# Kernel optimization log

Hardware: AMD Instinct MI355X
Metric: run time of the kernel (lower is better)

Reference implementation:

```python
import jax, jax.numpy as jnp
import numpy as np

N = 4096      # mesh nodes (seq len)
D = 512       # input_dim_nodes / hidden_size
F = 512       # ffn_hidden_size (hidden_dim)
NH = 4        # num_attention_heads
HD = D // NH  # head dim = 128
L = 2         # processor_layers
EPS = 1e-5
SCALE = 1.0 / float(np.sqrt(HD))
NEG = -1e9


def setup_inputs() -> dict:
    key = jax.random.key(0)
    ks = jax.random.split(key, 16)
    nfeat = jax.random.normal(ks[0], (N, D), jnp.float32)
    # sparse graph adjacency mask: True = masked out (TE 'arbitrary' convention)
    mask = jax.random.uniform(ks[1], (N, N)) < 0.99
    idx = jnp.arange(N)
    mask = mask.at[idx, idx].set(False)  # keep self-edges unmasked
    s = 0.02
    p = lambda k, shape: jax.random.normal(k, shape, jnp.float32) * s
    return dict(
        nfeat=nfeat, mask=mask,
        ln1_g=jnp.ones((L, D), jnp.float32), ln1_b=jnp.zeros((L, D), jnp.float32),
        wq=p(ks[2], (L, D, D)), bq=p(ks[3], (L, D)),
        wk=p(ks[4], (L, D, D)), bk=p(ks[5], (L, D)),
        wv=p(ks[6], (L, D, D)), bv=p(ks[7], (L, D)),
        wo=p(ks[8], (L, D, D)), bo=p(ks[9], (L, D)),
        ln2_g=jnp.ones((L, D), jnp.float32), ln2_b=jnp.zeros((L, D), jnp.float32),
        fc1_w=p(ks[10], (L, F, D)), fc1_b=p(ks[11], (L, F)),
        fc2_w=p(ks[12], (L, D, F)), fc2_b=p(ks[13], (L, D)),
    )


def _ln(x, g, b):
    mu = x.mean(-1, keepdims=True)
    var = ((x - mu) ** 2).mean(-1, keepdims=True)
    return (x - mu) * jax.lax.rsqrt(var + EPS) * g + b


def reference(nfeat, mask, ln1_g, ln1_b, wq, bq, wk, bk, wv, bv, wo, bo,
              ln2_g, ln2_b, fc1_w, fc1_b, fc2_w, fc2_b):
    def layer(x, p):
        g1, b1, Wq, Bq, Wk, Bk, Wv, Bv, Wo, Bo, g2, b2, W1, B1, W2, B2 = p
        # --- pre-LN self-attention with arbitrary mask ---
        h = _ln(x, g1, b1)                                  # [N, D]
        q = (h @ Wq.T + Bq).reshape(N, NH, HD)
        k = (h @ Wk.T + Bk).reshape(N, NH, HD)
        v = (h @ Wv.T + Bv).reshape(N, NH, HD)
        scores = jnp.einsum('qhd,khd->hqk', q, k) * SCALE   # [NH, N, N]
        scores = jnp.where(mask[None], NEG, scores)
        attn = jax.nn.softmax(scores, axis=-1)
        o = jnp.einsum('hqk,khd->qhd', attn, v).reshape(N, D)
        x = x + o @ Wo.T + Bo
        # --- pre-LN MLP ---
        h2 = _ln(x, g2, b2)
        m = jax.nn.gelu(h2 @ W1.T + B1, approximate=False) @ W2.T + B2
        return x + m, None

    xs = (ln1_g, ln1_b, wq, bq, wk, bk, wv, bv, wo, bo,
          ln2_g, ln2_b, fc1_w, fc1_b, fc2_w, fc2_b)
    out, _ = jax.lax.scan(layer, nfeat, xs)
    return out
```

## Files before the change

kernel.cpp:

```cpp
#include <hip/hip_runtime.h>
#include <math.h>

#define NN 4096
#define DD 512
#define FF 512
#define NHEAD 4
#define HDIM 128
#define CAP 256
#define SCALE 0.08838834764831845f

typedef __attribute__((ext_vector_type(8))) short short8;
typedef __attribute__((ext_vector_type(8))) unsigned short ushort8;
typedef __attribute__((ext_vector_type(4))) unsigned short ushort4v;
typedef __attribute__((ext_vector_type(4))) float floatx4;

__device__ __forceinline__ float bf2f(unsigned short u) {
    union { unsigned int i; float f; } x; x.i = ((unsigned int)u) << 16; return x.f;
}
__device__ __forceinline__ unsigned short f2bf(float f) {
    union { float f; unsigned int i; } x; x.f = f;
    unsigned int r = (x.i + 0x7FFFu + ((x.i >> 16) & 1u)) >> 16;
    return (unsigned short)r;
}
__device__ __forceinline__ void gld_lds16(const void* g, void* l) {
    __builtin_amdgcn_global_load_lds((const __attribute__((address_space(1))) void*)g,
                                     (__attribute__((address_space(3))) void*)l, 16, 0, 0);
}

__global__ void build_idx_kernel(const int* __restrict__ mask,
                                 int* __restrict__ idx, int* __restrict__ cnt) {
    int row = blockIdx.x;
    __shared__ int c;
    if (threadIdx.x == 0) c = 0;
    __syncthreads();
    const int4* mrow = (const int4*)(mask + (size_t)row * NN);
    for (int j4 = threadIdx.x; j4 < NN / 4; j4 += blockDim.x) {
        int4 m4 = mrow[j4];
        int base = j4 * 4;
        if (m4.x == 0) idx[row * CAP + atomicAdd(&c, 1)] = base;
        if (m4.y == 0) idx[row * CAP + atomicAdd(&c, 1)] = base + 1;
        if (m4.z == 0) idx[row * CAP + atomicAdd(&c, 1)] = base + 2;
        if (m4.w == 0) idx[row * CAP + atomicAdd(&c, 1)] = base + 3;
    }
    __syncthreads();
    if (threadIdx.x == 0) cnt[row] = (c < CAP) ? c : CAP;
}

struct W6 { const float* w[6]; };
__global__ void cast_weights(W6 wp, unsigned short* __restrict__ dst) {
    int region = blockIdx.x >> 4;
    int layer = region / 6, mat = region - layer * 6;
    const float* src = wp.w[mat] + (size_t)layer * (DD * DD);
    unsigned short* d = dst + (size_t)region * (DD * DD);
    int off = (blockIdx.x & 15) * 16384 + threadIdx.x * 4;
#pragma unroll
    for (int i = 0; i < 16; i++) {
        int e = off + i * 1024;
        float4 f = *(const float4*)&src[e];
        ushort4v u;
        u.x = f2bf(f.x); u.y = f2bf(f.y); u.z = f2bf(f.z); u.w = f2bf(f.w);
        *(ushort4v*)&d[e] = u;
    }
}

__global__ void concat_bias(const float* __restrict__ bq, const float* __restrict__ bk,
                            const float* __restrict__ bv, float* __restrict__ bcat) {
    int l = blockIdx.x, t = threadIdx.x;
    bcat[l * 1536 + t]        = bq[l * 512 + t];
    bcat[l * 1536 + 512 + t]  = bk[l * 512 + t];
    bcat[l * 1536 + 1024 + t] = bv[l * 512 + t];
}

__global__ void ln_kernel(const float* __restrict__ x, const float* __restrict__ g,
                          const float* __restrict__ b, unsigned short* __restrict__ out) {
    int wave = threadIdx.x >> 6, lane = threadIdx.x & 63;
    int row = blockIdx.x * 4 + wave;
    const float* xr = x + (size_t)row * DD;
    float v[8];
    float4 p0 = *(const float4*)&xr[lane * 8];
    float4 p1 = *(const float4*)&xr[lane * 8 + 4];
    v[0] = p0.x; v[1] = p0.y; v[2] = p0.z; v[3] = p0.w;
    v[4] = p1.x; v[5] = p1.y; v[6] = p1.z; v[7] = p1.w;
    float s = 0.f;
#pragma unroll
    for (int i = 0; i < 8; i++) s += v[i];
#pragma unroll
    for (int off = 32; off; off >>= 1) s += __shfl_xor(s, off);
    float mu = s * (1.0f / DD);
    float vs = 0.f;
#pragma unroll
    for (int i = 0; i < 8; i++) { float d = v[i] - mu; vs += d * d; }
#pragma unroll
    for (int off = 32; off; off >>= 1) vs += __shfl_xor(vs, off);
    float r = rsqrtf(vs * (1.0f / DD) + 1e-5f);
    float4 g0 = *(const float4*)&g[lane * 8];
    float4 g1 = *(const float4*)&g[lane * 8 + 4];
    float4 b0 = *(const float4*)&b[lane * 8];
    float4 b1 = *(const float4*)&b[lane * 8 + 4];
    float ge[8] = {g0.x, g0.y, g0.z, g0.w, g1.x, g1.y, g1.z, g1.w};
    float be[8] = {b0.x, b0.y, b0.z, b0.w, b1.x, b1.y, b1.z, b1.w};
    ushort8 ov;
#pragma unroll
    for (int i = 0; i < 8; i++) ov[i] = f2bf((v[i] - mu) * r * ge[i] + be[i]);
    *(ushort8*)&out[(size_t)row * DD + lane * 8] = ov;
}

template <int MODE>
__launch_bounds__(256)
__global__ void gemm_bf16(const unsigned short* __restrict__ A, const unsigned short* __restrict__ B,
                          const float* __restrict__ bias, const float* __restrict__ resIn,
                          float* __restrict__ resOut, unsigned short* __restrict__ outB,
                          int M, int Nout, int K) {
    __shared__ unsigned short As[64 * 32];
    __shared__ unsigned short Bs[64 * 32];
    const int m0 = blockIdx.y * 64, n0 = blockIdx.x * 64;
    const int t = threadIdx.x;
    const int wave = t >> 6, lane = t & 63;
    const int wm = (wave & 1) * 32, wn = (wave >> 1) * 32;
    const int srow = t >> 2, scol = (t & 3) * 8;
    const int fr = lane & 15, fq = (lane >> 4) * 8;

    floatx4 acc[2][2] = {};

    const unsigned short* ag = A + (size_t)(m0 + srow) * K + scol;
    const unsigned short* bg = B + (size_t)(n0 + srow) * K + scol;
    unsigned short* as = As + t * 8;
    unsigned short* bs = Bs + t * 8;

    for (int k0 = 0; k0 < K; k0 += 32) {
        __syncthreads();
        gld_lds16(ag + k0, as);
        gld_lds16(bg + k0, bs);
        __syncthreads();
        short8 af[2], bf[2];
#pragma unroll
        for (int i = 0; i < 2; i++)
            af[i] = *(const short8*)&As[(wm + 16 * i + fr) * 32 + fq];
#pragma unroll
        for (int j = 0; j < 2; j++)
            bf[j] = *(const short8*)&Bs[(wn + 16 * j + fr) * 32 + fq];
#pragma unroll
        for (int i = 0; i < 2; i++)
#pragma unroll
            for (int j = 0; j < 2; j++)
                acc[i][j] = __builtin_amdgcn_mfma_f32_16x16x32_bf16(af[i], bf[j], acc[i][j], 0, 0, 0);
    }

    const int er = (lane >> 4) * 4, ec = lane & 15;
#pragma unroll
    for (int i = 0; i < 2; i++) {
#pragma unroll
        for (int j = 0; j < 2; j++) {
            int col = n0 + wn + 16 * j + ec;
            float bsv = bias[col];
#pragma unroll
            for (int r = 0; r < 4; r++) {
                int row = m0 + wm + 16 * i + er + r;
                float val = acc[i][j][r] + bsv;
                if (MODE == 1) val = 0.5f * val * (1.0f + erff(val * 0.70710678118654752f));
                if (MODE == 2) {
                    resOut[(size_t)row * Nout + col] = resIn[(size_t)row * Nout + col] + val;
                } else {
                    outB[(size_t)row * Nout + col] = f2bf(val);
                }
            }
        }
    }
}

__global__ void sparse_attn(const unsigned short* __restrict__ qkv, const int* __restrict__ idx,
                            const int* __restrict__ cnt, unsigned short* __restrict__ o) {
    int wave = threadIdx.x >> 6, lane = threadIdx.x & 63;
    int qslot = wave >> 1, half = wave & 1;
    int qi = blockIdx.x * 4 + qslot;
    __shared__ float obuf[4][64][8];
    __shared__ float sbuf[4][64];

    ushort8 qv = *(const ushort8*)(qkv + (size_t)qi * 1536 + lane * 8);
    float qf[8];
#pragma unroll
    for (int e = 0; e < 8; e++) qf[e] = bf2f(qv[e]);

    int c = cnt[qi];
    const int* ir = idx + qi * CAP;
    float sum = 0.f, oa[8] = {};

    for (int j = half; j < c; j += 2) {
        int kj = ir[j];
        const unsigned short* kv_base = qkv + (size_t)kj * 1536;
        ushort8 kv = *(const ushort8*)(kv_base + 512 + lane * 8);
        ushort8 vv = *(const ushort8*)(kv_base + 1024 + lane * 8);
        float d = 0.f;
#pragma unroll
        for (int e = 0; e < 8; e++) d += qf[e] * bf2f(kv[e]);
        d += __shfl_xor(d, 1);
        d += __shfl_xor(d, 2);
        d += __shfl_xor(d, 4);
        d += __shfl_xor(d, 8);
        float p = __expf(d * SCALE);
        sum += p;
#pragma unroll
        for (int e = 0; e < 8; e++) oa[e] += p * bf2f(vv[e]);
    }

    if (half == 1) {
#pragma unroll
        for (int e = 0; e < 8; e++) obuf[qslot][lane][e] = oa[e];
        sbuf[qslot][lane] = sum;
    }
    __syncthreads();
    if (half == 0) {
        sum += sbuf[qslot][lane];
        float inv = 1.0f / sum;
        ushort8 ov;
#pragma unroll
        for (int e = 0; e < 8; e++) ov[e] = f2bf((oa[e] + obuf[qslot][lane][e]) * inv);
        *(ushort8*)(o + (size_t)qi * 512 + lane * 8) = ov;
    }
}

extern "C" void kernel_launch(void* const* d_in, const int* in_sizes, int n_in,
                              void* d_out, int out_size, void* d_ws, size_t ws_size,
                              hipStream_t stream) {
    const float* nfeat = (const float*)d_in[0];
    const int*   mask  = (const int*)d_in[1];
    const float* ln1_g = (const float*)d_in[2];
    const float* ln1_b = (const float*)d_in[3];
    const float* wq    = (const float*)d_in[4];
    const float* bq    = (const float*)d_in[5];
    const float* wk    = (const float*)d_in[6];
    const float* bk    = (const float*)d_in[7];
    const float* wv    = (const float*)d_in[8];
    const float* bv    = (const float*)d_in[9];
    const float* wo    = (const float*)d_in[10];
    const float* bo    = (const float*)d_in[11];
    const float* ln2_g = (const float*)d_in[12];
    const float* ln2_b = (const float*)d_in[13];
    const float* fc1_w = (const float*)d_in[14];
    const float* fc1_b = (const float*)d_in[15];
    const float* fc2_w = (const float*)d_in[16];
    const float* fc2_b = (const float*)d_in[17];

    const size_t ND = (size_t)NN * DD;
    float* x            = (float*)d_ws;
    unsigned short* h   = (unsigned short*)(x + ND);
    unsigned short* qkv = h + ND;
    unsigned short* o   = qkv + (size_t)NN * 1536;
    unsigned short* m1  = o + ND;
    unsigned short* wc  = m1 + ND;
    float* bcat         = (float*)(wc + (size_t)12 * DD * DD);
    int*   idx          = (int*)(bcat + 2 * 1536);
    int*   cnt          = idx + (size_t)NN * CAP;

    W6 w6;
    w6.w[0] = wq; w6.w[1] = wk; w6.w[2] = wv; w6.w[3] = wo; w6.w[4] = fc1_w; w6.w[5] = fc2_w;
    cast_weights<<<192, 256, 0, stream>>>(w6, wc);
    concat_bias<<<2, 512, 0, stream>>>(bq, bk, bv, bcat);
    build_idx_kernel<<<NN, 256, 0, stream>>>(mask, idx, cnt);

    for (int l = 0; l < 2; l++) {
        size_t bOff = (size_t)l * DD;
        unsigned short* wl = wc + (size_t)l * 6 * DD * DD;
        const float* xin = (l == 0) ? nfeat : x;
        float* fc2_dst = (l == 1) ? (float*)d_out : x;

        ln_kernel<<<NN / 4, 256, 0, stream>>>(xin, ln1_g + bOff, ln1_b + bOff, h);
        gemm_bf16<0><<<dim3(24, 64), 256, 0, stream>>>(h, wl, bcat + l * 1536, nullptr, nullptr, qkv, NN, 1536, DD);
        sparse_attn<<<NN / 4, 512, 0, stream>>>(qkv, idx, cnt, o);
        gemm_bf16<2><<<dim3(8, 64), 256, 0, stream>>>(o, wl + (size_t)3 * DD * DD, bo + bOff, xin, x, nullptr, NN, DD, DD);
        ln_kernel<<<NN / 4, 256, 0, stream>>>(x, ln2_g + bOff, ln2_b + bOff, h);
        gemm_bf16<1><<<dim3(8, 64), 256, 0, stream>>>(h, wl + (size_t)4 * DD * DD, fc1_b + bOff, nullptr, nullptr, m1, NN, FF, DD);
        gemm_bf16<2><<<dim3(8, 64), 256, 0, stream>>>(m1, wl + (size_t)5 * DD * DD, fc2_b + bOff, x, fc2_dst, nullptr, NN, DD, FF);
    }
}
```

Baseline: 309.4 us.

## Fold LayerNorm into GEMM weights and compute row stats in residual epilogues

Folds the LayerNorm gamma/beta into the bf16 QKV and FC1 weights, adding per-column constants c0/c1, so the standalone LN kernels disappear. Row sum and sum-of-squares come from an init kernel for the input and from atomics in the residual-GEMM epilogues, which also write a bf16 copy of x. The following GEMM then applies mean/rstd in its epilogue. This removes four LN launches and their extra passes over x, in exchange for atomics, a one-pass variance formula with possible cancellation error, and bf16 rounding of the unnormalized x.

```diff
diff --git a/kernel.cpp b/kernel.cpp
--- a/kernel.cpp
+++ b/kernel.cpp
@@ -4,14 +4,11 @@
 #define NN 4096
 #define DD 512
 #define FF 512
-#define NHEAD 4
-#define HDIM 128
 #define CAP 256
 #define SCALE 0.08838834764831845f
 
 typedef __attribute__((ext_vector_type(8))) short short8;
 typedef __attribute__((ext_vector_type(8))) unsigned short ushort8;
-typedef __attribute__((ext_vector_type(4))) unsigned short ushort4v;
 typedef __attribute__((ext_vector_type(4))) float floatx4;
 
 __device__ __forceinline__ float bf2f(unsigned short u) {
@@ -46,71 +43,91 @@
     if (threadIdx.x == 0) cnt[row] = (c < CAP) ? c : CAP;
 }
 
-struct W6 { const float* w[6]; };
-__global__ void cast_weights(W6 wp, unsigned short* __restrict__ dst) {
-    int region = blockIdx.x >> 4;
-    int layer = region / 6, mat = region - layer * 6;
-    const float* src = wp.w[mat] + (size_t)layer * (DD * DD);
-    unsigned short* d = dst + (size_t)region * (DD * DD);
-    int off = (blockIdx.x & 15) * 16384 + threadIdx.x * 4;
-#pragma unroll
-    for (int i = 0; i < 16; i++) {
-        int e = off + i * 1024;
-        float4 f = *(const float4*)&src[e];
-        ushort4v u;
-        u.x = f2bf(f.x); u.y = f2bf(f.y); u.z = f2bf(f.z); u.w = f2bf(f.w);
-        *(ushort4v*)&d[e] = u;
-    }
-}
-
-__global__ void concat_bias(const float* __restrict__ bq, const float* __restrict__ bk,
-                            const float* __restrict__ bv, float* __restrict__ bcat) {
-    int l = blockIdx.x, t = threadIdx.x;
-    bcat[l * 1536 + t]        = bq[l * 512 + t];
-    bcat[l * 1536 + 512 + t]  = bk[l * 512 + t];
-    bcat[l * 1536 + 1024 + t] = bv[l * 512 + t];
-}
-
-__global__ void ln_kernel(const float* __restrict__ x, const float* __restrict__ g,
-                          const float* __restrict__ b, unsigned short* __restrict__ out) {
+struct FoldArgs {
+    const float* w[6];
+    const float* bias[6];
+    const float* ln1_g; const float* ln1_b;
+    const float* ln2_g; const float* ln2_b;
+};
+__global__ void fold_weights(FoldArgs fa, unsigned short* __restrict__ wc,
+                             float* __restrict__ c0, float* __restrict__ c1) {
+    int r = blockIdx.y;
+    int l = r / 6, m = r - l * 6;
+    int wave = threadIdx.x >> 6, lane = threadIdx.x & 63;
+    int n = blockIdx.x * 4 + wave;
+
+    const float* wrow = fa.w[m] + (size_t)l * DD * DD + (size_t)n * DD;
+    float4 w0 = *(const float4*)&wrow[lane * 8];
+    float4 w1 = *(const float4*)&wrow[lane * 8 + 4];
+    float we[8] = {w0.x, w0.y, w0.z, w0.w, w1.x, w1.y, w1.z, w1.w};
+
+    bool folded = (m < 3) || (m == 4);
+    float s1 = 0.f, sb = 0.f;
+    float wg[8];
+    if (folded) {
+        const float* gp = (m < 3) ? fa.ln1_g + l * DD : fa.ln2_g + l * DD;
+        const float* bp = (m < 3) ? fa.ln1_b + l * DD : fa.ln2_b + l * DD;
+        float4 g0 = *(const float4*)&gp[lane * 8];
+        float4 g1 = *(const float4*)&gp[lane * 8 + 4];
+        float4 b0 = *(const float4*)&bp[lane * 8];
+        float4 b1 = *(const float4*)&bp[lane * 8 + 4];
+        float ge[8] = {g0.x, g0.y, g0.z, g0.w, g1.x, g1.y, g1.z, g1.w};
+        float be[8] = {b0.x, b0.y, b0.z, b0.w, b1.x, b1.y, b1.z, b1.w};
+#pragma unroll
+        for (int e = 0; e < 8; e++) {
+            wg[e] = we[e] * ge[e];
+            s1 += wg[e];
+            sb += we[e] * be[e];
+        }
+    } else {
+#pragma unroll
+        for (int e = 0; e < 8; e++) wg[e] = we[e];
+    }
+    ushort8 ov;
+#pragma unroll
+    for (int e = 0; e < 8; e++) ov[e] = f2bf(wg[e]);
+    *(ushort8*)&wc[(size_t)r * DD * DD + (size_t)n * DD + lane * 8] = ov;
+
+    if (folded) {
+#pragma unroll
+        for (int off = 32; off; off >>= 1) { s1 += __shfl_xor(s1, off); sb += __shfl_xor(sb, off); }
+    }
+    if (lane == 0) {
+        c1[r * DD + n] = folded ? s1 : 0.f;
+        c0[r * DD + n] = (folded ? sb : 0.f) + fa.bias[m][l * DD + n];
+    }
+}
+
+__global__ void init_stats(const float* __restrict__ x, unsigned short* __restrict__ xb,
+                           float* __restrict__ S) {
     int wave = threadIdx.x >> 6, lane = threadIdx.x & 63;
     int row = blockIdx.x * 4 + wave;
     const float* xr = x + (size_t)row * DD;
-    float v[8];
     float4 p0 = *(const float4*)&xr[lane * 8];
     float4 p1 = *(const float4*)&xr[lane * 8 + 4];
-    v[0] = p0.x; v[1] = p0.y; v[2] = p0.z; v[3] = p0.w;
-    v[4] = p1.x; v[5] = p1.y; v[6] = p1.z; v[7] = p1.w;
-    float s = 0.f;
-#pragma unroll
-    for (int i = 0; i < 8; i++) s += v[i];
-#pragma unroll
-    for (int off = 32; off; off >>= 1) s += __shfl_xor(s, off);
-    float mu = s * (1.0f / DD);
-    float vs = 0.f;
-#pragma unroll
-    for (int i = 0; i < 8; i++) { float d = v[i] - mu; vs += d * d; }
-#pragma unroll
-    for (int off = 32; off; off >>= 1) vs += __shfl_xor(vs, off);
-    float r = rsqrtf(vs * (1.0f / DD) + 1e-5f);
-    float4 g0 = *(const float4*)&g[lane * 8];
-    float4 g1 = *(const float4*)&g[lane * 8 + 4];
-    float4 b0 = *(const float4*)&b[lane * 8];
-    float4 b1 = *(const float4*)&b[lane * 8 + 4];
-    float ge[8] = {g0.x, g0.y, g0.z, g0.w, g1.x, g1.y, g1.z, g1.w};
-    float be[8] = {b0.x, b0.y, b0.z, b0.w, b1.x, b1.y, b1.z, b1.w};
+    float v[8] = {p0.x, p0.y, p0.z, p0.w, p1.x, p1.y, p1.z, p1.w};
+    float s = 0.f, q = 0.f;
     ushort8 ov;
 #pragma unroll
-    for (int i = 0; i < 8; i++) ov[i] = f2bf((v[i] - mu) * r * ge[i] + be[i]);
-    *(ushort8*)&out[(size_t)row * DD + lane * 8] = ov;
+    for (int e = 0; e < 8; e++) { s += v[e]; q += v[e] * v[e]; ov[e] = f2bf(v[e]); }
+#pragma unroll
+    for (int off = 32; off; off >>= 1) { s += __shfl_xor(s, off); q += __shfl_xor(q, off); }
+    *(ushort8*)&xb[(size_t)row * DD + lane * 8] = ov;
+    if (lane == 0) { S[2 * row] = s; S[2 * row + 1] = q; }
+}
+
+__global__ void zero_kernel(float* __restrict__ p, int n) {
+    int i = blockIdx.x * blockDim.x + threadIdx.x;
+    if (i < n) p[i] = 0.f;
 }
 
 template <int MODE>
 __launch_bounds__(256)
 __global__ void gemm_bf16(const unsigned short* __restrict__ A, const unsigned short* __restrict__ B,
-                          const float* __restrict__ bias, const float* __restrict__ resIn,
+                          const float* __restrict__ c0, const float* __restrict__ c1,
+                          const float* __restrict__ statsIn, const float* __restrict__ resIn,
                           float* __restrict__ resOut, unsigned short* __restrict__ outB,
-                          int M, int Nout, int K) {
+                          float* __restrict__ statsOut, int M, int Nout, int K) {
     __shared__ unsigned short As[64 * 32];
     __shared__ unsigned short Bs[64 * 32];
     const int m0 = blockIdx.y * 64, n0 = blockIdx.x * 64;
@@ -147,21 +164,51 @@
     }
 
     const int er = (lane >> 4) * 4, ec = lane & 15;
+    int colj[2]; float c0v[2], c1v[2];
+#pragma unroll
+    for (int j = 0; j < 2; j++) {
+        colj[j] = n0 + wn + 16 * j + ec;
+        c0v[j] = c0[colj[j]];
+        if (MODE < 2) c1v[j] = c1[colj[j]];
+    }
+
 #pragma unroll
     for (int i = 0; i < 2; i++) {
 #pragma unroll
-        for (int j = 0; j < 2; j++) {
-            int col = n0 + wn + 16 * j + ec;
-            float bsv = bias[col];
-#pragma unroll
-            for (int r = 0; r < 4; r++) {
-                int row = m0 + wm + 16 * i + er + r;
-                float val = acc[i][j][r] + bsv;
-                if (MODE == 1) val = 0.5f * val * (1.0f + erff(val * 0.70710678118654752f));
+        for (int r = 0; r < 4; r++) {
+            int row = m0 + wm + 16 * i + er + r;
+            if (MODE < 2) {
+                float s = statsIn[2 * row], q = statsIn[2 * row + 1];
+                float mu = s * (1.0f / DD);
+                float var = q * (1.0f / DD) - mu * mu;
+                float rm = rsqrtf(var + 1e-5f);
+                float rmu = rm * mu;
+#pragma unroll
+                for (int j = 0; j < 2; j++) {
+                    float val = rm * acc[i][j][r] - rmu * c1v[j] + c0v[j];
+                    if (MODE == 1) val = 0.5f * val * (1.0f + erff(val * 0.70710678118654752f));
+                    outB[(size_t)row * Nout + colj[j]] = f2bf(val);
+                }
+            } else {
+                float xn[2];
+#pragma unroll
+                for (int j = 0; j < 2; j++) {
+                    xn[j] = resIn[(size_t)row * Nout + colj[j]] + acc[i][j][r] + c0v[j];
+                    resOut[(size_t)row * Nout + colj[j]] = xn[j];
+                    if (MODE == 2) outB[(size_t)row * Nout + colj[j]] = f2bf(xn[j]);
+                }
                 if (MODE == 2) {
-                    resOut[(size_t)row * Nout + col] = resIn[(size_t)row * Nout + col] + val;
-                } else {
-                    outB[(size_t)row * Nout + col] = f2bf(val);
+                    float s = xn[0] + xn[1];
+                    float q = xn[0] * xn[0] + xn[1] * xn[1];
+#pragma unroll
+                    for (int off = 1; off < 16; off <<= 1) {
+                        s += __shfl_xor(s, off);
+                        q += __shfl_xor(q, off);
+                    }
+                    if ((lane & 15) == 0) {
+                        atomicAdd(&statsOut[2 * row], s);
+                        atomicAdd(&statsOut[2 * row + 1], q);
+                    }
                 }
             }
         }
@@ -243,33 +290,48 @@
 
     const size_t ND = (size_t)NN * DD;
     float* x            = (float*)d_ws;
-    unsigned short* h   = (unsigned short*)(x + ND);
-    unsigned short* qkv = h + ND;
+    unsigned short* xb  = (unsigned short*)(x + ND);
+    unsigned short* qkv = xb + ND;
     unsigned short* o   = qkv + (size_t)NN * 1536;
     unsigned short* m1  = o + ND;
     unsigned short* wc  = m1 + ND;
-    float* bcat         = (float*)(wc + (size_t)12 * DD * DD);
-    int*   idx          = (int*)(bcat + 2 * 1536);
+    float* c0           = (float*)(wc + (size_t)12 * DD * DD);
+    float* c1           = c0 + 12 * DD;
+    float* S            = c1 + 12 * DD;
+    int*   idx          = (int*)(S + 4 * NN * 2);
     int*   cnt          = idx + (size_t)NN * CAP;
 
-    W6 w6;
-    w6.w[0] = wq; w6.w[1] = wk; w6.w[2] = wv; w6.w[3] = wo; w6.w[4] = fc1_w; w6.w[5] = fc2_w;
-    cast_weights<<<192, 256, 0, stream>>>(w6, wc);
-    concat_bias<<<2, 512, 0, stream>>>(bq, bk, bv, bcat);
+    FoldArgs fa;
+    fa.w[0] = wq; fa.w[1] = wk; fa.w[2] = wv; fa.w[3] = wo; fa.w[4] = fc1_w; fa.w[5] = fc2_w;
+    fa.bias[0] = bq; fa.bias[1] = bk; fa.bias[2] = bv; fa.bias[3] = bo; fa.bias[4] = fc1_b; fa.bias[5] = fc2_b;
+    fa.ln1_g = ln1_g; fa.ln1_b = ln1_b; fa.ln2_g = ln2_g; fa.ln2_b = ln2_b;
+
+    fold_weights<<<dim3(128, 12), 256, 0, stream>>>(fa, wc, c0, c1);
     build_idx_kernel<<<NN, 256, 0, stream>>>(mask, idx, cnt);
+    init_stats<<<NN / 4, 256, 0, stream>>>(nfeat, xb, S);
+    zero_kernel<<<24, 1024, 0, stream>>>(S + NN * 2, 3 * NN * 2);
 
     for (int l = 0; l < 2; l++) {
-        size_t bOff = (size_t)l * DD;
         unsigned short* wl = wc + (size_t)l * 6 * DD * DD;
-        const float* xin = (l == 0) ? nfeat : x;
-        float* fc2_dst = (l == 1) ? (float*)d_out : x;
-
-        ln_kernel<<<NN / 4, 256, 0, stream>>>(xin, ln1_g + bOff, ln1_b + bOff, h);
-        gemm_bf16<0><<<dim3(24, 64), 256, 0, stream>>>(h, wl, bcat + l * 1536, nullptr, nullptr, qkv, NN, 1536, DD);
+        float* cl0 = c0 + l * 6 * DD;
+        float* cl1 = c1 + l * 6 * DD;
+        float* Sa = S + (size_t)(2 * l) * NN * 2;
+        float* Sb = S + (size_t)(2 * l + 1) * NN * 2;
+        const float* resIn0 = (l == 0) ? nfeat : x;
+
+        gemm_bf16<0><<<dim3(24, 64), 256, 0, stream>>>(xb, wl, cl0, cl1, Sa,
+                                                       nullptr, nullptr, qkv, nullptr, NN, 1536, DD);
         sparse_attn<<<NN / 4, 512, 0, stream>>>(qkv, idx, cnt, o);
-        gemm_bf16<2><<<dim3(8, 64), 256, 0, stream>>>(o, wl + (size_t)3 * DD * DD, bo + bOff, xin, x, nullptr, NN, DD, DD);
-        ln_kernel<<<NN / 4, 256, 0, stream>>>(x, ln2_g + bOff, ln2_b + bOff, h);
-        gemm_bf16<1><<<dim3(8, 64), 256, 0, stream>>>(h, wl + (size_t)4 * DD * DD, fc1_b + bOff, nullptr, nullptr, m1, NN, FF, DD);
-        gemm_bf16<2><<<dim3(8, 64), 256, 0, stream>>>(m1, wl + (size_t)5 * DD * DD, fc2_b + bOff, x, fc2_dst, nullptr, NN, DD, FF);
-    }
-}
+        gemm_bf16<2><<<dim3(8, 64), 256, 0, stream>>>(o, wl + (size_t)3 * DD * DD, cl0 + 3 * DD, nullptr,
+                                                      nullptr, resIn0, x, xb, Sb, NN, DD, DD);
+        gemm_bf16<1><<<dim3(8, 64), 256, 0, stream>>>(xb, wl + (size_t)4 * DD * DD, cl0 + 4 * DD, cl1 + 4 * DD, Sb,
+                                                      nullptr, nullptr, m1, nullptr, NN, FF, DD);
+        if (l == 0) {
+            gemm_bf16<2><<<dim3(8, 64), 256, 0, stream>>>(m1, wl + (size_t)5 * DD * DD, cl0 + 5 * DD, nullptr,
+                                                          nullptr, x, x, xb, S + (size_t)2 * NN * 2, NN, DD, FF);
+        } else {
+            gemm_bf16<3><<<dim3(8, 64), 256, 0, stream>>>(m1, wl + (size_t)5 * DD * DD, cl0 + 5 * DD, nullptr,
+                                                          nullptr, x, (float*)d_out, nullptr, nullptr, NN, DD, FF);
+        }
+    }
+}
```

Result: slower. 321.8 us (+4.0%).

## Enlarge GEMM tiles and merge setup kernels into one launch

Applied to the files above, without the earlier changes.

The GEMM kernel now uses 128-row tiles with either 128 or 64 columns (templated NJ), so each wave computes a 64xN block with more MFMAs per LDS load and fewer blocks are launched. The weight cast, bias concat and mask-to-index build are folded into a single setup kernel that handles 8 mask rows per block, which cuts launch count and the per-row block overhead. The index build also gains a bounds check on CAP. The larger tiles raise register and LDS use per block and halve the grid size, which may reduce occupancy and load balance.

```diff
diff --git a/kernel.cpp b/kernel.cpp
--- a/kernel.cpp
+++ b/kernel.cpp
@@ -4,83 +4,91 @@
 #define NN 4096
 #define DD 512
 #define FF 512
-#define NHEAD 4
-#define HDIM 128
 #define CAP 256
 #define SCALE 0.08838834764831845f
 
+typedef unsigned short u16;
 typedef __attribute__((ext_vector_type(8))) short short8;
 typedef __attribute__((ext_vector_type(8))) unsigned short ushort8;
 typedef __attribute__((ext_vector_type(4))) unsigned short ushort4v;
 typedef __attribute__((ext_vector_type(4))) float floatx4;
 
-__device__ __forceinline__ float bf2f(unsigned short u) {
+__device__ __forceinline__ float bf2f(u16 u) {
     union { unsigned int i; float f; } x; x.i = ((unsigned int)u) << 16; return x.f;
 }
-__device__ __forceinline__ unsigned short f2bf(float f) {
+__device__ __forceinline__ u16 f2bf(float f) {
     union { float f; unsigned int i; } x; x.f = f;
     unsigned int r = (x.i + 0x7FFFu + ((x.i >> 16) & 1u)) >> 16;
-    return (unsigned short)r;
+    return (u16)r;
 }
 __device__ __forceinline__ void gld_lds16(const void* g, void* l) {
     __builtin_amdgcn_global_load_lds((const __attribute__((address_space(1))) void*)g,
                                      (__attribute__((address_space(3))) void*)l, 16, 0, 0);
 }
 
-__global__ void build_idx_kernel(const int* __restrict__ mask,
-                                 int* __restrict__ idx, int* __restrict__ cnt) {
-    int row = blockIdx.x;
-    __shared__ int c;
-    if (threadIdx.x == 0) c = 0;
+struct SetupArgs {
+    const float* w[6];
+    const float* bq; const float* bk; const float* bv;
+    const int* mask;
+    u16* wc; float* bcat; int* idx; int* cnt;
+};
+__global__ void setup_kernel(SetupArgs a) {
+    const int bid = blockIdx.x, t = threadIdx.x;
+    const int wave = t >> 6, lane = t & 63;
+    __shared__ int cbar[8];
+
+    for (int it = 0; it < 3; it++) {
+        int gid = bid * 3 + it;
+        int r = gid >> 7, nb = gid & 127;
+        int l = r / 6, m = r - l * 6;
+        int n = nb * 4 + wave;
+        const float* src = a.w[m] + (size_t)l * DD * DD + (size_t)n * DD;
+        float4 w0 = *(const float4*)&src[lane * 8];
+        float4 w1 = *(const float4*)&src[lane * 8 + 4];
+        float we[8] = {w0.x, w0.y, w0.z, w0.w, w1.x, w1.y, w1.z, w1.w};
+        ushort8 ov;
+#pragma unroll
+        for (int e = 0; e < 8; e++) ov[e] = f2bf(we[e]);
+        *(ushort8*)&a.wc[(size_t)r * DD * DD + (size_t)n * DD + lane * 8] = ov;
+    }
+
+    if (bid == 0) {
+        for (int l = 0; l < 2; l++)
+            for (int it = 0; it < 6; it++) {
+                int j = it * 256 + t;
+                int m = j >> 9, col = j & 511;
+                const float* bp = (m == 0) ? a.bq : (m == 1) ? a.bk : a.bv;
+                a.bcat[l * 1536 + j] = bp[l * DD + col];
+            }
+    }
+
+    if (t < 8) cbar[t] = 0;
     __syncthreads();
-    const int4* mrow = (const int4*)(mask + (size_t)row * NN);
-    for (int j4 = threadIdx.x; j4 < NN / 4; j4 += blockDim.x) {
-        int4 m4 = mrow[j4];
-        int base = j4 * 4;
-        if (m4.x == 0) idx[row * CAP + atomicAdd(&c, 1)] = base;
-        if (m4.y == 0) idx[row * CAP + atomicAdd(&c, 1)] = base + 1;
-        if (m4.z == 0) idx[row * CAP + atomicAdd(&c, 1)] = base + 2;
-        if (m4.w == 0) idx[row * CAP + atomicAdd(&c, 1)] = base + 3;
+    for (int h = 0; h < 2; h++) {
+        int rr = wave * 2 + h;
+        int row = bid * 8 + rr;
+        const int4* mr = (const int4*)(a.mask + (size_t)row * NN);
+        for (int j4 = lane; j4 < NN / 4; j4 += 64) {
+            int4 m4 = mr[j4];
+            int base = j4 * 4;
+            if (m4.x == 0) { int p = atomicAdd(&cbar[rr], 1); if (p < CAP) a.idx[row * CAP + p] = base; }
+            if (m4.y == 0) { int p = atomicAdd(&cbar[rr], 1); if (p < CAP) a.idx[row * CAP + p] = base + 1; }
+            if (m4.z == 0) { int p = atomicAdd(&cbar[rr], 1); if (p < CAP) a.idx[row * CAP + p] = base + 2; }
+            if (m4.w == 0) { int p = atomicAdd(&cbar[rr], 1); if (p < CAP) a.idx[row * CAP + p] = base + 3; }
+        }
     }
     __syncthreads();
-    if (threadIdx.x == 0) cnt[row] = (c < CAP) ? c : CAP;
-}
-
-struct W6 { const float* w[6]; };
-__global__ void cast_weights(W6 wp, unsigned short* __restrict__ dst) {
-    int region = blockIdx.x >> 4;
-    int layer = region / 6, mat = region - layer * 6;
-    const float* src = wp.w[mat] + (size_t)layer * (DD * DD);
-    unsigned short* d = dst + (size_t)region * (DD * DD);
-    int off = (blockIdx.x & 15) * 16384 + threadIdx.x * 4;
-#pragma unroll
-    for (int i = 0; i < 16; i++) {
-        int e = off + i * 1024;
-        float4 f = *(const float4*)&src[e];
-        ushort4v u;
-        u.x = f2bf(f.x); u.y = f2bf(f.y); u.z = f2bf(f.z); u.w = f2bf(f.w);
-        *(ushort4v*)&d[e] = u;
-    }
-}
-
-__global__ void concat_bias(const float* __restrict__ bq, const float* __restrict__ bk,
-                            const float* __restrict__ bv, float* __restrict__ bcat) {
-    int l = blockIdx.x, t = threadIdx.x;
-    bcat[l * 1536 + t]        = bq[l * 512 + t];
-    bcat[l * 1536 + 512 + t]  = bk[l * 512 + t];
-    bcat[l * 1536 + 1024 + t] = bv[l * 512 + t];
+    if (t < 8) { int c = cbar[t]; a.cnt[bid * 8 + t] = (c < CAP) ? c : CAP; }
 }
 
 __global__ void ln_kernel(const float* __restrict__ x, const float* __restrict__ g,
-                          const float* __restrict__ b, unsigned short* __restrict__ out) {
+                          const float* __restrict__ b, u16* __restrict__ out) {
     int wave = threadIdx.x >> 6, lane = threadIdx.x & 63;
     int row = blockIdx.x * 4 + wave;
     const float* xr = x + (size_t)row * DD;
-    float v[8];
     float4 p0 = *(const float4*)&xr[lane * 8];
     float4 p1 = *(const float4*)&xr[lane * 8 + 4];
-    v[0] = p0.x; v[1] = p0.y; v[2] = p0.z; v[3] = p0.w;
-    v[4] = p1.x; v[5] = p1.y; v[6] = p1.z; v[7] = p1.w;
+    float v[8] = {p0.x, p0.y, p0.z, p0.w, p1.x, p1.y, p1.z, p1.w};
     float s = 0.f;
 #pragma unroll
     for (int i = 0; i < 8; i++) s += v[i];
@@ -105,71 +113,81 @@
     *(ushort8*)&out[(size_t)row * DD + lane * 8] = ov;
 }
 
-template <int MODE>
+template <int MODE, int NJ>
 __launch_bounds__(256)
-__global__ void gemm_bf16(const unsigned short* __restrict__ A, const unsigned short* __restrict__ B,
+__global__ void gemm_bf16(const u16* __restrict__ A, const u16* __restrict__ B,
                           const float* __restrict__ bias, const float* __restrict__ resIn,
-                          float* __restrict__ resOut, unsigned short* __restrict__ outB,
-                          int M, int Nout, int K) {
-    __shared__ unsigned short As[64 * 32];
-    __shared__ unsigned short Bs[64 * 32];
-    const int m0 = blockIdx.y * 64, n0 = blockIdx.x * 64;
+                          float* __restrict__ resOut, u16* __restrict__ outB, int Nout) {
+    constexpr int TN = NJ * 32;
+    __shared__ u16 As[128 * 32];
+    __shared__ u16 Bs[TN * 32];
+    const int m0 = blockIdx.y * 128, n0 = blockIdx.x * TN;
     const int t = threadIdx.x;
     const int wave = t >> 6, lane = t & 63;
-    const int wm = (wave & 1) * 32, wn = (wave >> 1) * 32;
+    const int wm = (wave & 1) * 64, wn = (wave >> 1) * (TN / 2);
     const int srow = t >> 2, scol = (t & 3) * 8;
     const int fr = lane & 15, fq = (lane >> 4) * 8;
 
-    floatx4 acc[2][2] = {};
-
-    const unsigned short* ag = A + (size_t)(m0 + srow) * K + scol;
-    const unsigned short* bg = B + (size_t)(n0 + srow) * K + scol;
-    unsigned short* as = As + t * 8;
-    unsigned short* bs = Bs + t * 8;
-
-    for (int k0 = 0; k0 < K; k0 += 32) {
+    floatx4 acc[4][NJ] = {};
+
+    const u16* ag0 = A + (size_t)(m0 + srow) * DD + scol;
+    const u16* ag1 = ag0 + (size_t)64 * DD;
+    const u16* bg0 = B + (size_t)(n0 + srow) * DD + scol;
+    const u16* bg1 = bg0 + (size_t)64 * DD;
+    u16* as0 = As + t * 8;
+    u16* as1 = as0 + 64 * 32;
+    u16* bs0 = Bs + t * 8;
+    u16* bs1 = bs0 + 64 * 32;
+
+    for (int k0 = 0; k0 < DD; k0 += 32) {
         __syncthreads();
-        gld_lds16(ag + k0, as);
-        gld_lds16(bg + k0, bs);
+        gld_lds16(ag0 + k0, as0);
+        gld_lds16(ag1 + k0, as1);
+        gld_lds16(bg0 + k0, bs0);
+        if (NJ == 4) gld_lds16(bg1 + k0, bs1);
         __syncthreads();
-        short8 af[2], bf[2];
-#pragma unroll
-        for (int i = 0; i < 2; i++)
+        short8 af[4], bf[NJ];
+#pragma unroll
+        for (int i = 0; i < 4; i++)
             af[i] = *(const short8*)&As[(wm + 16 * i + fr) * 32 + fq];
 #pragma unroll
-        for (int j = 0; j < 2; j++)
+        for (int j = 0; j < NJ; j++)
             bf[j] = *(const short8*)&Bs[(wn + 16 * j + fr) * 32 + fq];
 #pragma unroll
-        for (int i = 0; i < 2; i++)
-#pragma unroll
-            for (int j = 0; j < 2; j++)
+        for (int i = 0; i < 4; i++)
+#pragma unroll
+            for (int j = 0; j < NJ; j++)
                 acc[i][j] = __builtin_amdgcn_mfma_f32_16x16x32_bf16(af[i], bf[j], acc[i][j], 0, 0, 0);
     }
 
     const int er = (lane >> 4) * 4, ec = lane & 15;
-#pragma unroll
-    for (int i = 0; i < 2; i++) {
-#pragma unroll
-        for (int j = 0; j < 2; j++) {
-            int col = n0 + wn + 16 * j + ec;
-            float bsv = bias[col];
-#pragma unroll
-            for (int r = 0; r < 4; r++) {
-                int row = m0 + wm + 16 * i + er + r;
-                float val = acc[i][j][r] + bsv;
+    int colj[NJ]; float bv[NJ];
+#pragma unroll
+    for (int j = 0; j < NJ; j++) {
+        colj[j] = n0 + wn + 16 * j + ec;
+        bv[j] = bias[colj[j]];
+    }
+#pragma unroll
+    for (int i = 0; i < 4; i++) {
+#pragma unroll
+        for (int r = 0; r < 4; r++) {
+            int row = m0 + wm + 16 * i + er + r;
+#pragma unroll
+            for (int j = 0; j < NJ; j++) {
+                float val = acc[i][j][r] + bv[j];
                 if (MODE == 1) val = 0.5f * val * (1.0f + erff(val * 0.70710678118654752f));
                 if (MODE == 2) {
-                    resOut[(size_t)row * Nout + col] = resIn[(size_t)row * Nout + col] + val;
+                    resOut[(size_t)row * Nout + colj[j]] = resIn[(size_t)row * Nout + colj[j]] + val;
                 } else {
-                    outB[(size_t)row * Nout + col] = f2bf(val);
+                    outB[(size_t)row * Nout + colj[j]] = f2bf(val);
                 }
             }
         }
     }
 }
 
-__global__ void sparse_attn(const unsigned short* __restrict__ qkv, const int* __restrict__ idx,
-                            const int* __restrict__ cnt, unsigned short* __restrict__ o) {
+__global__ void sparse_attn(const u16* __restrict__ qkv, const int* __restrict__ idx,
+                            const int* __restrict__ cnt, u16* __restrict__ o) {
     int wave = threadIdx.x >> 6, lane = threadIdx.x & 63;
     int qslot = wave >> 1, half = wave & 1;
     int qi = blockIdx.x * 4 + qslot;
@@ -187,7 +205,7 @@
 
     for (int j = half; j < c; j += 2) {
         int kj = ir[j];
-        const unsigned short* kv_base = qkv + (size_t)kj * 1536;
+        const u16* kv_base = qkv + (size_t)kj * 1536;
         ushort8 kv = *(const ushort8*)(kv_base + 512 + lane * 8);
         ushort8 vv = *(const ushort8*)(kv_base + 1024 + lane * 8);
         float d = 0.f;
@@ -226,50 +244,49 @@
     const int*   mask  = (const int*)d_in[1];
     const float* ln1_g = (const float*)d_in[2];
     const float* ln1_b = (const float*)d_in[3];
-    const float* wq    = (const float*)d_in[4];
-    const float* bq    = (const float*)d_in[5];
-    const float* wk    = (const float*)d_in[6];
-    const float* bk    = (const float*)d_in[7];
-    const float* wv    = (const float*)d_in[8];
-    const float* bv    = (const float*)d_in[9];
-    const float* wo    = (const float*)d_in[10];
     const float* bo    = (const float*)d_in[11];
     const float* ln2_g = (const float*)d_in[12];
     const float* ln2_b = (const float*)d_in[13];
-    const float* fc1_w = (const float*)d_in[14];
     const float* fc1_b = (const float*)d_in[15];
-    const float* fc2_w = (const float*)d_in[16];
     const float* fc2_b = (const float*)d_in[17];
 
     const size_t ND = (size_t)NN * DD;
-    float* x            = (float*)d_ws;
-    unsigned short* h   = (unsigned short*)(x + ND);
-    unsigned short* qkv = h + ND;
-    unsigned short* o   = qkv + (size_t)NN * 1536;
-    unsigned short* m1  = o + ND;
-    unsigned short* wc  = m1 + ND;
-    float* bcat         = (float*)(wc + (size_t)12 * DD * DD);
-    int*   idx          = (int*)(bcat + 2 * 1536);
-    int*   cnt          = idx + (size_t)NN * CAP;
-
-    W6 w6;
-    w6.w[0] = wq; w6.w[1] = wk; w6.w[2] = wv; w6.w[3] = wo; w6.w[4] = fc1_w; w6.w[5] = fc2_w;
-    cast_weights<<<192, 256, 0, stream>>>(w6, wc);
-    concat_bias<<<2, 512, 0, stream>>>(bq, bk, bv, bcat);
-    build_idx_kernel<<<NN, 256, 0, stream>>>(mask, idx, cnt);
-
+    float* x   = (float*)d_ws;
+    u16*   h   = (u16*)(x + ND);
+    u16*   qkv = h + ND;
+    u16*   o   = qkv + (size_t)NN * 1536;
+    u16*   m1  = o + ND;
+    u16*   wc  = m1 + ND;
+    float* bcat = (float*)(wc + (size_t)12 * DD * DD);
+    int*   idx  = (int*)(bcat + 2 * 1536);
+    int*   cnt  = idx + (size_t)NN * CAP;
+
+    SetupArgs sa;
+    sa.w[0] = (const float*)d_in[4];  sa.w[1] = (const float*)d_in[6];
+    sa.w[2] = (const float*)d_in[8];  sa.w[3] = (const float*)d_in[10];
+    sa.w[4] = (const float*)d_in[14]; sa.w[5] = (const float*)d_in[16];
+    sa.bq = (const float*)d_in[5]; sa.bk = (const float*)d_in[7]; sa.bv = (const float*)d_in[9];
+    sa.mask = mask; sa.wc = wc; sa.bcat = bcat; sa.idx = idx; sa.cnt = cnt;
+
+    setup_kernel<<<512, 256, 0, stream>>>(sa);
+
+    const size_t SS = (size_t)DD * DD;
     for (int l = 0; l < 2; l++) {
         size_t bOff = (size_t)l * DD;
-        unsigned short* wl = wc + (size_t)l * 6 * DD * DD;
+        u16* wl = wc + (size_t)l * 6 * SS;
         const float* xin = (l == 0) ? nfeat : x;
         float* fc2_dst = (l == 1) ? (float*)d_out : x;
 
         ln_kernel<<<NN / 4, 256, 0, stream>>>(xin, ln1_g + bOff, ln1_b + bOff, h);
-        gemm_bf16<0><<<dim3(24, 64), 256, 0, stream>>>(h, wl, bcat + l * 1536, nullptr, nullptr, qkv, NN, 1536, DD);
+        gemm_bf16<0, 4><<<dim3(12, 32), 256, 0, stream>>>(h, wl, bcat + l * 1536,
+                                                          nullptr, nullptr, qkv, 1536);
         sparse_attn<<<NN / 4, 512, 0, stream>>>(qkv, idx, cnt, o);
-        gemm_bf16<2><<<dim3(8, 64), 256, 0, stream>>>(o, wl + (size_t)3 * DD * DD, bo + bOff, xin, x, nullptr, NN, DD, DD);
+        gemm_bf16<2, 2><<<dim3(8, 32), 256, 0, stream>>>(o, wl + 3 * SS, bo + bOff,
+                                                         xin, x, nullptr, DD);
         ln_kernel<<<NN / 4, 256, 0, stream>>>(x, ln2_g + bOff, ln2_b + bOff, h);
-        gemm_bf16<1><<<dim3(8, 64), 256, 0, stream>>>(h, wl + (size_t)4 * DD * DD, fc1_b + bOff, nullptr, nullptr, m1, NN, FF, DD);
-        gemm_bf16<2><<<dim3(8, 64), 256, 0, stream>>>(m1, wl + (size_t)5 * DD * DD, fc2_b + bOff, x, fc2_dst, nullptr, NN, DD, FF);
-    }
-}
+        gemm_bf16<1, 2><<<dim3(8, 32), 256, 0, stream>>>(h, wl + 4 * SS, fc1_b + bOff,
+                                                         nullptr, nullptr, m1, FF);
+        gemm_bf16<2, 2><<<dim3(8, 32), 256, 0, stream>>>(m1, wl + 5 * SS, fc2_b + bOff,
+                                                         x, fc2_dst, nullptr, DD);
+    }
+}
```

Result: slower. 343.1 us (+10.9%).

## Prefetch next K/V rows in sparse attention and use 128-row QKV GEMM tiles

Applied to the files above, without the earlier changes.

The sparse attention kernel now stages each query's neighbour index list in shared memory and software-pipelines the K/V gathers, loading the next neighbour's K and V rows while computing on the current ones. This hides gather latency at the cost of extra registers. A dedicated QKV GEMM kernel with 128x64 tiles halves the block count and reuses each B tile across more rows, which lowers LDS and global traffic per MFMA.

```diff
diff --git a/kernel.cpp b/kernel.cpp
--- a/kernel.cpp
+++ b/kernel.cpp
@@ -4,23 +4,22 @@
 #define NN 4096
 #define DD 512
 #define FF 512
-#define NHEAD 4
-#define HDIM 128
 #define CAP 256
 #define SCALE 0.08838834764831845f
 
+typedef unsigned short u16;
 typedef __attribute__((ext_vector_type(8))) short short8;
 typedef __attribute__((ext_vector_type(8))) unsigned short ushort8;
 typedef __attribute__((ext_vector_type(4))) unsigned short ushort4v;
 typedef __attribute__((ext_vector_type(4))) float floatx4;
 
-__device__ __forceinline__ float bf2f(unsigned short u) {
+__device__ __forceinline__ float bf2f(u16 u) {
     union { unsigned int i; float f; } x; x.i = ((unsigned int)u) << 16; return x.f;
 }
-__device__ __forceinline__ unsigned short f2bf(float f) {
+__device__ __forceinline__ u16 f2bf(float f) {
     union { float f; unsigned int i; } x; x.f = f;
     unsigned int r = (x.i + 0x7FFFu + ((x.i >> 16) & 1u)) >> 16;
-    return (unsigned short)r;
+    return (u16)r;
 }
 __device__ __forceinline__ void gld_lds16(const void* g, void* l) {
     __builtin_amdgcn_global_load_lds((const __attribute__((address_space(1))) void*)g,
@@ -47,11 +46,11 @@
 }
 
 struct W6 { const float* w[6]; };
-__global__ void cast_weights(W6 wp, unsigned short* __restrict__ dst) {
+__global__ void cast_weights(W6 wp, u16* __restrict__ dst) {
     int region = blockIdx.x >> 4;
     int layer = region / 6, mat = region - layer * 6;
     const float* src = wp.w[mat] + (size_t)layer * (DD * DD);
-    unsigned short* d = dst + (size_t)region * (DD * DD);
+    u16* d = dst + (size_t)region * (DD * DD);
     int off = (blockIdx.x & 15) * 16384 + threadIdx.x * 4;
 #pragma unroll
     for (int i = 0; i < 16; i++) {
@@ -72,15 +71,13 @@
 }
 
 __global__ void ln_kernel(const float* __restrict__ x, const float* __restrict__ g,
-                          const float* __restrict__ b, unsigned short* __restrict__ out) {
+                          const float* __restrict__ b, u16* __restrict__ out) {
     int wave = threadIdx.x >> 6, lane = threadIdx.x & 63;
     int row = blockIdx.x * 4 + wave;
     const float* xr = x + (size_t)row * DD;
-    float v[8];
     float4 p0 = *(const float4*)&xr[lane * 8];
     float4 p1 = *(const float4*)&xr[lane * 8 + 4];
-    v[0] = p0.x; v[1] = p0.y; v[2] = p0.z; v[3] = p0.w;
-    v[4] = p1.x; v[5] = p1.y; v[6] = p1.z; v[7] = p1.w;
+    float v[8] = {p0.x, p0.y, p0.z, p0.w, p1.x, p1.y, p1.z, p1.w};
     float s = 0.f;
 #pragma unroll
     for (int i = 0; i < 8; i++) s += v[i];
@@ -107,12 +104,12 @@
 
 template <int MODE>
 __launch_bounds__(256)
-__global__ void gemm_bf16(const unsigned short* __restrict__ A, const unsigned short* __restrict__ B,
+__global__ void gemm_bf16(const u16* __restrict__ A, const u16* __restrict__ B,
                           const float* __restrict__ bias, const float* __restrict__ resIn,
-                          float* __restrict__ resOut, unsigned short* __restrict__ outB,
+                          float* __restrict__ resOut, u16* __restrict__ outB,
                           int M, int Nout, int K) {
-    __shared__ unsigned short As[64 * 32];
-    __shared__ unsigned short Bs[64 * 32];
+    __shared__ u16 As[64 * 32];
+    __shared__ u16 Bs[64 * 32];
     const int m0 = blockIdx.y * 64, n0 = blockIdx.x * 64;
     const int t = threadIdx.x;
     const int wave = t >> 6, lane = t & 63;
@@ -121,11 +118,10 @@
     const int fr = lane & 15, fq = (lane >> 4) * 8;
 
     floatx4 acc[2][2] = {};
-
-    const unsigned short* ag = A + (size_t)(m0 + srow) * K + scol;
-    const unsigned short* bg = B + (size_t)(n0 + srow) * K + scol;
-    unsigned short* as = As + t * 8;
-    unsigned short* bs = Bs + t * 8;
+    const u16* ag = A + (size_t)(m0 + srow) * K + scol;
+    const u16* bg = B + (size_t)(n0 + srow) * K + scol;
+    u16* as = As + t * 8;
+    u16* bs = Bs + t * 8;
 
     for (int k0 = 0; k0 < K; k0 += 32) {
         __syncthreads();
@@ -134,11 +130,9 @@
         __syncthreads();
         short8 af[2], bf[2];
 #pragma unroll
-        for (int i = 0; i < 2; i++)
-            af[i] = *(const short8*)&As[(wm + 16 * i + fr) * 32 + fq];
-#pragma unroll
-        for (int j = 0; j < 2; j++)
-            bf[j] = *(const short8*)&Bs[(wn + 16 * j + fr) * 32 + fq];
+        for (int i = 0; i < 2; i++) af[i] = *(const short8*)&As[(wm + 16 * i + fr) * 32 + fq];
+#pragma unroll
+        for (int j = 0; j < 2; j++) bf[j] = *(const short8*)&Bs[(wn + 16 * j + fr) * 32 + fq];
 #pragma unroll
         for (int i = 0; i < 2; i++)
 #pragma unroll
@@ -168,28 +162,97 @@
     }
 }
 
-__global__ void sparse_attn(const unsigned short* __restrict__ qkv, const int* __restrict__ idx,
-                            const int* __restrict__ cnt, unsigned short* __restrict__ o) {
-    int wave = threadIdx.x >> 6, lane = threadIdx.x & 63;
+__launch_bounds__(256)
+__global__ void gemm_qkv(const u16* __restrict__ A, const u16* __restrict__ B,
+                         const float* __restrict__ bias, u16* __restrict__ outB) {
+    __shared__ u16 As[128 * 32];
+    __shared__ u16 Bs[64 * 32];
+    const int m0 = blockIdx.y * 128, n0 = blockIdx.x * 64;
+    const int t = threadIdx.x;
+    const int wave = t >> 6, lane = t & 63;
+    const int wm = (wave & 1) * 64, wn = (wave >> 1) * 32;
+    const int srow = t >> 2, scol = (t & 3) * 8;
+    const int fr = lane & 15, fq = (lane >> 4) * 8;
+
+    floatx4 acc[4][2] = {};
+    const u16* ag0 = A + (size_t)(m0 + srow) * DD + scol;
+    const u16* ag1 = ag0 + (size_t)64 * DD;
+    const u16* bg = B + (size_t)(n0 + srow) * DD + scol;
+    u16* as0 = As + t * 8;
+    u16* as1 = as0 + 64 * 32;
+    u16* bs = Bs + t * 8;
+
+    for (int k0 = 0; k0 < DD; k0 += 32) {
+        __syncthreads();
+        gld_lds16(ag0 + k0, as0);
+        gld_lds16(ag1 + k0, as1);
+        gld_lds16(bg + k0, bs);
+        __syncthreads();
+        short8 af[4], bf[2];
+#pragma unroll
+        for (int i = 0; i < 4; i++) af[i] = *(const short8*)&As[(wm + 16 * i + fr) * 32 + fq];
+#pragma unroll
+        for (int j = 0; j < 2; j++) bf[j] = *(const short8*)&Bs[(wn + 16 * j + fr) * 32 + fq];
+#pragma unroll
+        for (int i = 0; i < 4; i++)
+#pragma unroll
+            for (int j = 0; j < 2; j++)
+                acc[i][j] = __builtin_amdgcn_mfma_f32_16x16x32_bf16(af[i], bf[j], acc[i][j], 0, 0, 0);
+    }
+
+    const int er = (lane >> 4) * 4, ec = lane & 15;
+#pragma unroll
+    for (int j = 0; j < 2; j++) {
+        int col = n0 + wn + 16 * j + ec;
+        float bsv = bias[col];
+#pragma unroll
+        for (int i = 0; i < 4; i++) {
+#pragma unroll
+            for (int r = 0; r < 4; r++) {
+                int row = m0 + wm + 16 * i + er + r;
+                outB[(size_t)row * 1536 + col] = f2bf(acc[i][j][r] + bsv);
+            }
+        }
+    }
+}
+
+__global__ void sparse_attn(const u16* __restrict__ qkv, const int* __restrict__ idx,
+                            const int* __restrict__ cnt, u16* __restrict__ o) {
+    int t = threadIdx.x;
+    int wave = t >> 6, lane = t & 63;
     int qslot = wave >> 1, half = wave & 1;
     int qi = blockIdx.x * 4 + qslot;
     __shared__ float obuf[4][64][8];
     __shared__ float sbuf[4][64];
+    __shared__ int sidx[4][CAP];
+
+    int c = cnt[qi];
+    const int* ir = idx + qi * CAP;
+    for (int j = t & 127; j < c; j += 128) sidx[qslot][j] = ir[j];
 
     ushort8 qv = *(const ushort8*)(qkv + (size_t)qi * 1536 + lane * 8);
     float qf[8];
 #pragma unroll
     for (int e = 0; e < 8; e++) qf[e] = bf2f(qv[e]);
-
-    int c = cnt[qi];
-    const int* ir = idx + qi * CAP;
+    __syncthreads();
+
     float sum = 0.f, oa[8] = {};
-
-    for (int j = half; j < c; j += 2) {
-        int kj = ir[j];
-        const unsigned short* kv_base = qkv + (size_t)kj * 1536;
-        ushort8 kv = *(const ushort8*)(kv_base + 512 + lane * 8);
-        ushort8 vv = *(const ushort8*)(kv_base + 1024 + lane * 8);
+    int j = half;
+    ushort8 kv, vv;
+    if (j < c) {
+        const u16* kb = qkv + (size_t)sidx[qslot][j] * 1536;
+        kv = *(const ushort8*)(kb + 512 + lane * 8);
+        vv = *(const ushort8*)(kb + 1024 + lane * 8);
+    }
+    while (j < c) {
+        int jn = j + 2;
+        ushort8 kvn, vvn;
+        {
+            int kjn = (jn < c) ? sidx[qslot][jn] : 0;
+            const u16* nb = qkv + (size_t)kjn * 1536;
+            kvn = *(const ushort8*)(nb + 512 + lane * 8);
+            vvn = *(const ushort8*)(nb + 1024 + lane * 8);
+        }
         float d = 0.f;
 #pragma unroll
         for (int e = 0; e < 8; e++) d += qf[e] * bf2f(kv[e]);
@@ -201,6 +264,8 @@
         sum += p;
 #pragma unroll
         for (int e = 0; e < 8; e++) oa[e] += p * bf2f(vv[e]);
+        kv = kvn; vv = vvn;
+        j = jn;
     }
 
     if (half == 1) {
@@ -226,50 +291,48 @@
     const int*   mask  = (const int*)d_in[1];
     const float* ln1_g = (const float*)d_in[2];
     const float* ln1_b = (const float*)d_in[3];
-    const float* wq    = (const float*)d_in[4];
-    const float* bq    = (const float*)d_in[5];
-    const float* wk    = (const float*)d_in[6];
-    const float* bk    = (const float*)d_in[7];
-    const float* wv    = (const float*)d_in[8];
-    const float* bv    = (const float*)d_in[9];
-    const float* wo    = (const float*)d_in[10];
     const float* bo    = (const float*)d_in[11];
     const float* ln2_g = (const float*)d_in[12];
     const float* ln2_b = (const float*)d_in[13];
-    const float* fc1_w = (const float*)d_in[14];
     const float* fc1_b = (const float*)d_in[15];
-    const float* fc2_w = (const float*)d_in[16];
     const float* fc2_b = (const float*)d_in[17];
 
     const size_t ND = (size_t)NN * DD;
-    float* x            = (float*)d_ws;
-    unsigned short* h   = (unsigned short*)(x + ND);
-    unsigned short* qkv = h + ND;
-    unsigned short* o   = qkv + (size_t)NN * 1536;
-    unsigned short* m1  = o + ND;
-    unsigned short* wc  = m1 + ND;
-    float* bcat         = (float*)(wc + (size_t)12 * DD * DD);
-    int*   idx          = (int*)(bcat + 2 * 1536);
-    int*   cnt          = idx + (size_t)NN * CAP;
+    float* x    = (float*)d_ws;
+    u16*   h    = (u16*)(x + ND);
+    u16*   qkv  = h + ND;
+    u16*   o    = qkv + (size_t)NN * 1536;
+    u16*   m1   = o + ND;
+    u16*   wc   = m1 + ND;
+    float* bcat = (float*)(wc + (size_t)12 * DD * DD);
+    int*   idx  = (int*)(bcat + 2 * 1536);
+    int*   cnt  = idx + (size_t)NN * CAP;
 
     W6 w6;
-    w6.w[0] = wq; w6.w[1] = wk; w6.w[2] = wv; w6.w[3] = wo; w6.w[4] = fc1_w; w6.w[5] = fc2_w;
+    w6.w[0] = (const float*)d_in[4];  w6.w[1] = (const float*)d_in[6];
+    w6.w[2] = (const float*)d_in[8];  w6.w[3] = (const float*)d_in[10];
+    w6.w[4] = (const float*)d_in[14]; w6.w[5] = (const float*)d_in[16];
     cast_weights<<<192, 256, 0, stream>>>(w6, wc);
-    concat_bias<<<2, 512, 0, stream>>>(bq, bk, bv, bcat);
+    concat_bias<<<2, 512, 0, stream>>>((const float*)d_in[5], (const float*)d_in[7],
+                                       (const float*)d_in[9], bcat);
     build_idx_kernel<<<NN, 256, 0, stream>>>(mask, idx, cnt);
 
+    const size_t SS = (size_t)DD * DD;
     for (int l = 0; l < 2; l++) {
         size_t bOff = (size_t)l * DD;
-        unsigned short* wl = wc + (size_t)l * 6 * DD * DD;
+        u16* wl = wc + (size_t)l * 6 * SS;
         const float* xin = (l == 0) ? nfeat : x;
         float* fc2_dst = (l == 1) ? (float*)d_out : x;
 
         ln_kernel<<<NN / 4, 256, 0, stream>>>(xin, ln1_g + bOff, ln1_b + bOff, h);
-        gemm_bf16<0><<<dim3(24, 64), 256, 0, stream>>>(h, wl, bcat + l * 1536, nullptr, nullptr, qkv, NN, 1536, DD);
+        gemm_qkv<<<dim3(24, 32), 256, 0, stream>>>(h, wl, bcat + l * 1536, qkv);
         sparse_attn<<<NN / 4, 512, 0, stream>>>(qkv, idx, cnt, o);
-        gemm_bf16<2><<<dim3(8, 64), 256, 0, stream>>>(o, wl + (size_t)3 * DD * DD, bo + bOff, xin, x, nullptr, NN, DD, DD);
+        gemm_bf16<2><<<dim3(8, 64), 256, 0, stream>>>(o, wl + 3 * SS, bo + bOff,
+                                                      xin, x, nullptr, NN, DD, DD);
         ln_kernel<<<NN / 4, 256, 0, stream>>>(x, ln2_g + bOff, ln2_b + bOff, h);
-        gemm_bf16<1><<<dim3(8, 64), 256, 0, stream>>>(h, wl + (size_t)4 * DD * DD, fc1_b + bOff, nullptr, nullptr, m1, NN, FF, DD);
-        gemm_bf16<2><<<dim3(8, 64), 256, 0, stream>>>(m1, wl + (size_t)5 * DD * DD, fc2_b + bOff, x, fc2_dst, nullptr, NN, DD, FF);
-    }
-}
+        gemm_bf16<1><<<dim3(8, 64), 256, 0, stream>>>(h, wl + 4 * SS, fc1_b + bOff,
+                                                      nullptr, nullptr, m1, NN, FF, DD);
+        gemm_bf16<2><<<dim3(8, 64), 256, 0, stream>>>(m1, wl + 5 * SS, fc2_b + bOff,
+                                                      x, fc2_dst, nullptr, NN, DD, FF);
+    }
+}
```

After: 293.6 us. 5.1% less time.
